# Kernel optimization log

Measured on AMD Instinct MI355X. Metric: run time of the kernel, lower is better.

## Reference

```python
import jax, jax.numpy as jnp
import numpy as np

B, S, E = 2, 2048, 2048
H, DH = 16, 128          # n_head, head_dim
ROT = 32                 # rotary_dim (partial RoPE)
MP = 8                   # mp_num in original forward
MASKED_BIAS = -1e9


def setup_inputs() -> dict:
    key = jax.random.key(0)
    k1, k2, k3 = jax.random.split(key, 3)
    hidden_states = jax.random.normal(k1, (B, S, E), dtype=jnp.float32)
    W_qkv = jax.random.normal(k2, (3 * E, E), dtype=jnp.float32) * (E ** -0.5)
    W_out = jax.random.normal(k3, (E, E), dtype=jnp.float32) * (E ** -0.5)
    return {"hidden_states": hidden_states, "W_qkv": W_qkv, "W_out": W_out}


def _rope_sincos(seq_len, rot_dim, dtype):
    inv_freq = 1.0 / (10000.0 ** (jnp.arange(0, rot_dim, 2, dtype=jnp.float32) / rot_dim))
    ang = jnp.arange(seq_len, dtype=jnp.float32)[:, None] * inv_freq[None, :]  # [S, R/2]
    return jnp.sin(ang).astype(dtype), jnp.cos(ang).astype(dtype)


def _apply_rope(x, sin, cos):
    # x: [B,S,H,R]; sin/cos: [S,R/2] -> repeat_interleave(2) -> [S,R]
    sin2 = jnp.repeat(sin, 2, axis=-1)[None, :, None, :]
    cos2 = jnp.repeat(cos, 2, axis=-1)[None, :, None, :]
    x1 = x[..., ::2]
    x2 = x[..., 1::2]
    rot = jnp.stack((-x2, x1), axis=-1).reshape(x.shape)  # rotate_every_two
    return x * cos2 + rot * sin2


def reference(hidden_states, W_qkv, W_out):
    b, s, e = hidden_states.shape
    # qkv_proj (no bias): torch Linear does x @ W^T
    qkv = jnp.einsum('bse,fe->bsf', hidden_states, W_qkv)          # [B,S,3E]
    qkv = qkv.reshape(b, s, MP, 3 * e // MP)
    q, k, v = jnp.split(qkv, 3, axis=-1)                            # each [B,S,MP,E/MP]
    # _split_heads: flatten mp dim, re-split into heads
    q = q.reshape(b, s, H, DH)
    k = k.reshape(b, s, H, DH)
    v = v.reshape(b, s, H, DH)
    # partial rotary on first ROT dims (q,k in [B,S,H,DH] layout)
    sin, cos = _rope_sincos(s, ROT, hidden_states.dtype)
    q = jnp.concatenate([_apply_rope(q[..., :ROT], sin, cos), q[..., ROT:]], axis=-1)
    k = jnp.concatenate([_apply_rope(k[..., :ROT], sin, cos), k[..., ROT:]], axis=-1)
    # attention: scores / sqrt(DH), causal masked_fill(-1e9), softmax, AV
    scale = jnp.sqrt(jnp.asarray(DH, dtype=jnp.float32)).astype(hidden_states.dtype)
    scores = jnp.einsum('bqhd,bkhd->bhqk', q, k) / scale            # [B,H,S,S]
    causal = jnp.tril(jnp.ones((s, s), dtype=bool))
    scores = jnp.where(causal[None, None], scores, jnp.asarray(MASKED_BIAS, scores.dtype))
    attn = jax.nn.softmax(scores, axis=-1)
    out = jnp.einsum('bhqk,bkhd->bqhd', attn, v)                    # [B,S,H,DH]
    out = out.reshape(b, s, e)
    return jnp.einsum('bse,fe->bsf', out, W_out)                    # out_proj
```

## Files before the change

kernel.cpp:

```cpp
#include <hip/hip_runtime.h>
#include <hip/hip_bf16.h>
#include <cstdint>
#include <cstddef>

using bf16 = __hip_bfloat16;
using short4v = __attribute__((ext_vector_type(4))) short;
using short8 = __attribute__((ext_vector_type(8))) short;
using floatx4 = __attribute__((ext_vector_type(4))) float;

#define MFMA_BF16(A, B, C) __builtin_amdgcn_mfma_f32_16x16x32_bf16((A), (B), (C), 0, 0, 0)

__device__ inline short bf16_bits(float x) {
  bf16 v = __float2bfloat16(x);
  short r;
  __builtin_memcpy(&r, &v, 2);
  return r;
}

__device__ inline void store_c(bf16* p, float v) { *p = __float2bfloat16(v); }
__device__ inline void store_c(float* p, float v) { *p = v; }

__global__ __launch_bounds__(256) void f32_to_bf16_kernel(
    const float* __restrict__ src, bf16* __restrict__ dst, int n8) {
  const int i = blockIdx.x * 256 + threadIdx.x;
  if (i >= n8) return;
  const float4 a = ((const float4*)src)[2 * i];
  const float4 b = ((const float4*)src)[2 * i + 1];
  short8 r;
  r[0] = bf16_bits(a.x); r[1] = bf16_bits(a.y); r[2] = bf16_bits(a.z); r[3] = bf16_bits(a.w);
  r[4] = bf16_bits(b.x); r[5] = bf16_bits(b.y); r[6] = bf16_bits(b.z); r[7] = bf16_bits(b.w);
  *(short8*)(dst + (size_t)i * 8) = r;
}

template <typename TC>
__global__ __launch_bounds__(256) void gemm_bt_async(
    const bf16* __restrict__ A, const bf16* __restrict__ B, TC* __restrict__ C,
    int ldc, int K) {
  __shared__ bf16 As[128 * 64];
  __shared__ bf16 Bs[128 * 64];
  const int tid = threadIdx.x;
  const int lane = tid & 63;
  const int wave = tid >> 6;
  const int lrow = lane & 15;
  const int quad = lane >> 4;
  const int wm = (wave >> 1) * 64;
  const int wn = (wave & 1) * 64;
  const int tm = blockIdx.y * 128;
  const int tn = blockIdx.x * 128;

  const int srow = tid >> 3;
  const int scl = tid & 7;

  floatx4 acc[4][4] = {};

  for (int k0 = 0; k0 < K; k0 += 64) {
    __syncthreads();
#pragma unroll
    for (int r = 0; r < 4; ++r) {
      const int row = r * 32 + srow;
      const int scg = scl ^ (row & 7);
      __builtin_amdgcn_global_load_lds(
          (const __attribute__((address_space(1))) void*)(A + (size_t)(tm + row) * K + k0 + scg * 8),
          (__attribute__((address_space(3))) void*)(As + row * 64 + scl * 8), 16, 0, 0);
    }
#pragma unroll
    for (int r = 0; r < 4; ++r) {
      const int row = r * 32 + srow;
      const int scg = scl ^ (row & 7);
      __builtin_amdgcn_global_load_lds(
          (const __attribute__((address_space(1))) void*)(B + (size_t)(tn + row) * K + k0 + scg * 8),
          (__attribute__((address_space(3))) void*)(Bs + row * 64 + scl * 8), 16, 0, 0);
    }
    __syncthreads();

#pragma unroll
    for (int kk = 0; kk < 2; ++kk) {
      short8 af[4], bfr[4];
#pragma unroll
      for (int i = 0; i < 4; ++i) {
        const int ra = wm + i * 16 + lrow;
        const int rb = wn + i * 16 + lrow;
        af[i] = *(const short8*)&As[ra * 64 + (((kk * 4 + quad) ^ (ra & 7)) * 8)];
        bfr[i] = *(const short8*)&Bs[rb * 64 + (((kk * 4 + quad) ^ (rb & 7)) * 8)];
      }
#pragma unroll
      for (int i = 0; i < 4; ++i)
#pragma unroll
        for (int j = 0; j < 4; ++j)
          acc[i][j] = MFMA_BF16(af[i], bfr[j], acc[i][j]);
    }
  }

#pragma unroll
  for (int i = 0; i < 4; ++i)
#pragma unroll
    for (int j = 0; j < 4; ++j)
#pragma unroll
      for (int r = 0; r < 4; ++r) {
        const int row = tm + wm + i * 16 + quad * 4 + r;
        const int col = tn + wn + j * 16 + lrow;
        store_c(&C[(size_t)row * ldc + col], acc[i][j][r]);
      }
}

__global__ __launch_bounds__(256) void gemm_abf16_bf32(
    const bf16* __restrict__ A, const float* __restrict__ B, float* __restrict__ C,
    int ldc, int K) {
  __shared__ bf16 As[128 * 64];
  __shared__ bf16 Bs[128 * 64];
  const int tid = threadIdx.x;
  const int lane = tid & 63;
  const int wave = tid >> 6;
  const int lrow = lane & 15;
  const int quad = lane >> 4;
  const int wm = (wave >> 1) * 64;
  const int wn = (wave & 1) * 64;
  const int tm = blockIdx.y * 128;
  const int tn = blockIdx.x * 128;

  const int srow = tid >> 3;
  const int scl = tid & 7;
  const int c16 = tid & 15;
  const int br0 = tid >> 4;

  floatx4 acc[4][4] = {};
  float4 breg[8];
#pragma unroll
  for (int r = 0; r < 8; ++r)
    breg[r] = *(const float4*)(B + (size_t)(tn + r * 16 + br0) * K + c16 * 4);

  for (int k0 = 0; k0 < K; k0 += 64) {
    __syncthreads();
#pragma unroll
    for (int r = 0; r < 4; ++r) {
      const int row = r * 32 + srow;
      const int scg = scl ^ (row & 7);
      __builtin_amdgcn_global_load_lds(
          (const __attribute__((address_space(1))) void*)(A + (size_t)(tm + row) * K + k0 + scg * 8),
          (__attribute__((address_space(3))) void*)(As + row * 64 + scl * 8), 16, 0, 0);
    }
#pragma unroll
    for (int r = 0; r < 8; ++r) {
      const int row = r * 16 + br0;
      short4v sv;
      sv[0] = bf16_bits(breg[r].x); sv[1] = bf16_bits(breg[r].y);
      sv[2] = bf16_bits(breg[r].z); sv[3] = bf16_bits(breg[r].w);
      *(short4v*)&Bs[row * 64 + (((c16 >> 1) ^ (row & 7)) * 8) + (c16 & 1) * 4] = sv;
    }
    __syncthreads();
    if (k0 + 64 < K) {
#pragma unroll
      for (int r = 0; r < 8; ++r)
        breg[r] = *(const float4*)(B + (size_t)(tn + r * 16 + br0) * K + k0 + 64 + c16 * 4);
    }

#pragma unroll
    for (int kk = 0; kk < 2; ++kk) {
      short8 af[4], bfr[4];
#pragma unroll
      for (int i = 0; i < 4; ++i) {
        const int ra = wm + i * 16 + lrow;
        const int rb = wn + i * 16 + lrow;
        af[i] = *(const short8*)&As[ra * 64 + (((kk * 4 + quad) ^ (ra & 7)) * 8)];
        bfr[i] = *(const short8*)&Bs[rb * 64 + (((kk * 4 + quad) ^ (rb & 7)) * 8)];
      }
#pragma unroll
      for (int i = 0; i < 4; ++i)
#pragma unroll
        for (int j = 0; j < 4; ++j)
          acc[i][j] = MFMA_BF16(af[i], bfr[j], acc[i][j]);
    }
  }

#pragma unroll
  for (int i = 0; i < 4; ++i)
#pragma unroll
    for (int j = 0; j < 4; ++j)
#pragma unroll
      for (int r = 0; r < 4; ++r) {
        const int row = tm + wm + i * 16 + quad * 4 + r;
        const int col = tn + wn + j * 16 + lrow;
        C[(size_t)row * ldc + col] = acc[i][j][r];
      }
}

__global__ void rope_kernel(bf16* __restrict__ qkv) {
  const int idx = blockIdx.x * 256 + threadIdx.x;
  const int i = idx & 15;
  int t = idx >> 4;
  const int qk = t & 1;
  t >>= 1;
  const int h = t & 15;
  t >>= 4;
  const int s = t & 2047;
  bf16* p = qkv + (size_t)t * 6144 + (h >> 1) * 768 + (h & 1) * 128 + qk * 256 + 2 * i;
  const float x0 = __bfloat162float(p[0]);
  const float x1 = __bfloat162float(p[1]);
  const float inv = powf(10000.f, -(float)(2 * i) / 32.f);
  const float ang = (float)s * inv;
  float sn, cs;
  sincosf(ang, &sn, &cs);
  p[0] = __float2bfloat16(x0 * cs - x1 * sn);
  p[1] = __float2bfloat16(x1 * cs + x0 * sn);
}

__global__ __launch_bounds__(256) void attn_flash_pair(
    const bf16* __restrict__ qkv, bf16* __restrict__ out) {
  __shared__ short Ks[16 * 64 * 8];
  __shared__ short Vs[8 * 128 * 8];
  __shared__ short Ps[8 * 128 * 8];
  const int tid = threadIdx.x;
  const int wave = tid >> 6;
  const int lane = tid & 63;
  const int lq = lane & 15;
  const int quad = lane >> 4;
  const int h = blockIdx.y;
  const int b = blockIdx.z;
  const size_t SROW = 6144;
  const bf16* base = qkv + (size_t)b * 2048 * SROW;
  const int qoff = (h >> 1) * 768 + (h & 1) * 128;
  const int koff = qoff + 256;
  const int voff = qoff + 512;
  const float scale = 0.088388347648318447f;

  const int sr = tid >> 2;
  const int sq = tid & 3;

  const bf16* kbase = base + (size_t)sr * SROW + koff + sq * 32;
  const bf16* vbase = base + (size_t)sr * SROW + voff + sq * 8;

  short8 kv[4], vv[4];
#pragma unroll
  for (int j = 0; j < 4; ++j) kv[j] = *(const short8*)(kbase + j * 8);
#pragma unroll
  for (int i = 0; i < 4; ++i) vv[i] = *(const short8*)(vbase + i * 32);

  for (int phase = 0; phase < 2; ++phase) {
    const int qb = phase ? (15 - (int)blockIdx.x) : (int)blockIdx.x;

    short8 qf[2][4];
#pragma unroll
    for (int rt = 0; rt < 2; ++rt) {
      const bf16* qp =
          base + (size_t)(qb * 128 + wave * 32 + rt * 16 + lq) * SROW + qoff + quad * 8;
#pragma unroll
      for (int ks = 0; ks < 4; ++ks) qf[rt][ks] = *(const short8*)(qp + ks * 32);
    }

    floatx4 o[2][8] = {};
    float m_i[2] = {-1e30f, -1e30f};
    float l_i[2] = {0.f, 0.f};

    const int kb_end = 2 * qb + 2;
    for (int kb = 0; kb < kb_end; ++kb) {
      __syncthreads();

#pragma unroll
      for (int j = 0; j < 4; ++j) *(short8*)&Ks[((sq * 4 + j) * 64 + sr) * 8] = kv[j];
      {
        const int so = (sr >> 3) * 128, si = sr & 7;
#pragma unroll
        for (int i = 0; i < 4; ++i) {
          const int d0 = sq * 8 + i * 32;
#pragma unroll
          for (int j = 0; j < 8; ++j) Vs[(so + d0 + j) * 8 + si] = vv[i][j];
        }
      }
      __syncthreads();

      {
        const bool last = (kb + 1 == kb_end);
        const bool pf = !last || (phase == 0);
        const int nkb = !last ? kb + 1 : 0;
        if (pf) {
          const size_t off = (size_t)nkb * 64 * SROW;
#pragma unroll
          for (int j = 0; j < 4; ++j) kv[j] = *(const short8*)(kbase + off + j * 8);
#pragma unroll
          for (int i = 0; i < 4; ++i) vv[i] = *(const short8*)(vbase + off + i * 32);
        }
      }

      floatx4 sc[2][4] = {};
      __builtin_amdgcn_s_setprio(1);
#pragma unroll
      for (int ks = 0; ks < 4; ++ks) {
        short8 kf[4];
#pragma unroll
        for (int ct = 0; ct < 4; ++ct)
          kf[ct] = *(const short8*)&Ks[((ks * 4 + quad) * 64 + ct * 16 + lq) * 8];
#pragma unroll
        for (int rt = 0; rt < 2; ++rt)
#pragma unroll
          for (int ct = 0; ct < 4; ++ct)
            sc[rt][ct] = MFMA_BF16(kf[ct], qf[rt][ks], sc[rt][ct]);
      }
      __builtin_amdgcn_s_setprio(0);

      const int qrow0 = qb * 128 + wave * 32;
      const bool diag = (kb * 64 + 63 > qrow0);
#pragma unroll
      for (int rt = 0; rt < 2; ++rt) {
        const int qg = qrow0 + rt * 16 + lq;
#pragma unroll
        for (int ct = 0; ct < 4; ++ct)
#pragma unroll
          for (int r = 0; r < 4; ++r) {
            float v = sc[rt][ct][r] * scale;
            if (diag && (kb * 64 + ct * 16 + quad * 4 + r) > qg) v = -1e9f;
            sc[rt][ct][r] = v;
          }
        float c0 = fmaxf(fmaxf(sc[rt][0][0], sc[rt][0][1]), fmaxf(sc[rt][0][2], sc[rt][0][3]));
        float c1 = fmaxf(fmaxf(sc[rt][1][0], sc[rt][1][1]), fmaxf(sc[rt][1][2], sc[rt][1][3]));
        float c2 = fmaxf(fmaxf(sc[rt][2][0], sc[rt][2][1]), fmaxf(sc[rt][2][2], sc[rt][2][3]));
        float c3 = fmaxf(fmaxf(sc[rt][3][0], sc[rt][3][1]), fmaxf(sc[rt][3][2], sc[rt][3][3]));
        float mx = fmaxf(fmaxf(c0, c1), fmaxf(c2, c3));
        mx = fmaxf(mx, __shfl_xor(mx, 16, 64));
        mx = fmaxf(mx, __shfl_xor(mx, 32, 64));
        const float mnew = fmaxf(m_i[rt], mx);
        const float alpha = __expf(m_i[rt] - mnew);
        m_i[rt] = mnew;
        float s0 = 0.f, s1 = 0.f, s2 = 0.f, s3 = 0.f;
#pragma unroll
        for (int ct = 0; ct < 4; ++ct) {
          const float p0 = __expf(sc[rt][ct][0] - mnew);
          const float p1 = __expf(sc[rt][ct][1] - mnew);
          const float p2 = __expf(sc[rt][ct][2] - mnew);
          const float p3 = __expf(sc[rt][ct][3] - mnew);
          sc[rt][ct][0] = p0; sc[rt][ct][1] = p1; sc[rt][ct][2] = p2; sc[rt][ct][3] = p3;
          s0 += p0; s1 += p1; s2 += p2; s3 += p3;
        }
        float rs = (s0 + s1) + (s2 + s3);
        rs += __shfl_xor(rs, 16, 64);
        rs += __shfl_xor(rs, 32, 64);
        l_i[rt] = l_i[rt] * alpha + rs;
#pragma unroll
        for (int dt = 0; dt < 8; ++dt) {
          o[rt][dt][0] *= alpha; o[rt][dt][1] *= alpha;
          o[rt][dt][2] *= alpha; o[rt][dt][3] *= alpha;
        }
        const int prow = wave * 32 + rt * 16 + lq;
#pragma unroll
        for (int ct = 0; ct < 4; ++ct) {
          short4v pv;
          pv[0] = bf16_bits(sc[rt][ct][0]); pv[1] = bf16_bits(sc[rt][ct][1]);
          pv[2] = bf16_bits(sc[rt][ct][2]); pv[3] = bf16_bits(sc[rt][ct][3]);
          const int kgrp = ct * 2 + (quad >> 1);
          *(short4v*)&Ps[(kgrp * 128 + prow) * 8 + (quad & 1) * 4] = pv;
        }
      }

      __builtin_amdgcn_s_setprio(1);
#pragma unroll
      for (int kk = 0; kk < 2; ++kk) {
        short8 pf[2], vf[8];
#pragma unroll
        for (int rt = 0; rt < 2; ++rt)
          pf[rt] = *(const short8*)&Ps[((kk * 4 + quad) * 128 + wave * 32 + rt * 16 + lq) * 8];
#pragma unroll
        for (int dt = 0; dt < 8; ++dt)
          vf[dt] = *(const short8*)&Vs[((kk * 4 + quad) * 128 + dt * 16 + lq) * 8];
#pragma unroll
        for (int rt = 0; rt < 2; ++rt)
#pragma unroll
          for (int dt = 0; dt < 8; ++dt)
            o[rt][dt] = MFMA_BF16(vf[dt], pf[rt], o[rt][dt]);
      }
      __builtin_amdgcn_s_setprio(0);
    }

#pragma unroll
    for (int rt = 0; rt < 2; ++rt) {
      const float inv_l = 1.f / l_i[rt];
      const int qg = qb * 128 + wave * 32 + rt * 16 + lq;
      bf16* op = out + ((size_t)(b * 2048 + qg)) * 2048 + h * 128 + quad * 4;
#pragma unroll
      for (int dt = 0; dt < 8; ++dt) {
        short4v s4;
        s4[0] = bf16_bits(o[rt][dt][0] * inv_l);
        s4[1] = bf16_bits(o[rt][dt][1] * inv_l);
        s4[2] = bf16_bits(o[rt][dt][2] * inv_l);
        s4[3] = bf16_bits(o[rt][dt][3] * inv_l);
        *(short4v*)(op + dt * 16) = s4;
      }
    }
  }
}

extern "C" void kernel_launch(void* const* d_in, const int* in_sizes, int n_in,
                              void* d_out, int out_size, void* d_ws, size_t ws_size,
                              hipStream_t stream) {
  const float* hidden = (const float*)d_in[0];
  const float* Wqkv = (const float*)d_in[1];
  const float* Wout = (const float*)d_in[2];
  float* outp = (float*)d_out;

  bf16* qkv = (bf16*)d_ws;
  bf16* flex = qkv + (size_t)4096 * 6144;
  bf16* hbf = (bf16*)d_out;

  f32_to_bf16_kernel<<<4096, 256, 0, stream>>>(hidden, hbf, 1048576);

  f32_to_bf16_kernel<<<3072, 256, 0, stream>>>(Wqkv, flex, 786432);
  gemm_bt_async<bf16><<<dim3(24, 32), 256, 0, stream>>>(hbf, flex, qkv, 6144, 2048);
  f32_to_bf16_kernel<<<3072, 256, 0, stream>>>(Wqkv + (size_t)3072 * 2048, flex, 786432);
  gemm_bt_async<bf16><<<dim3(24, 32), 256, 0, stream>>>(hbf, flex, qkv + 3072, 6144, 2048);

  rope_kernel<<<8192, 256, 0, stream>>>(qkv);

  bf16* attnout = flex;
  attn_flash_pair<<<dim3(8, 16, 2), 256, 0, stream>>>(qkv, attnout);

  gemm_abf16_bf32<<<dim3(16, 32), 256, 0, stream>>>(attnout, Wout, outp, 2048, 2048);
}
```

Before: 434.8 us.

## Write V transposed from QKV GEMM epilogue and skip no-op softmax rescaling

The QKV projection epilogue now writes the V columns into a separate head-major, transposed buffer ([b,h,d,s]) in the unused half of the output allocation. The attention kernel then loads V rows contiguously and stores them into shared memory with vector stores, replacing the scattered per-element LDS transpose. The online softmax also skips the alpha rescale of the accumulator and the row sum when no lane's max increased, gated by a wave-wide vote. The costs are strided 8-byte global stores in the GEMM epilogue and a divergent branch in the softmax.

Measured after the change: 435.4 us. No clear change (+0.1%).

```diff
diff --git a/kernel.cpp b/kernel.cpp
--- a/kernel.cpp
+++ b/kernel.cpp
@@ -35,7 +35,7 @@
 template <typename TC>
 __global__ __launch_bounds__(256) void gemm_bt_async(
     const bf16* __restrict__ A, const bf16* __restrict__ B, TC* __restrict__ C,
-    int ldc, int K) {
+    int ldc, int K, bf16* __restrict__ vT, int mpbase) {
   __shared__ bf16 As[128 * 64];
   __shared__ bf16 Bs[128 * 64];
   const int tid = threadIdx.x;
@@ -91,16 +91,36 @@
     }
   }
 
-#pragma unroll
-  for (int i = 0; i < 4; ++i)
-#pragma unroll
-    for (int j = 0; j < 4; ++j)
-#pragma unroll
-      for (int r = 0; r < 4; ++r) {
-        const int row = tm + wm + i * 16 + quad * 4 + r;
-        const int col = tn + wn + j * 16 + lrow;
-        store_c(&C[(size_t)row * ldc + col], acc[i][j][r]);
-      }
+  if (vT != nullptr && ((int)blockIdx.x % 6) >= 4) {
+    const int mpl = (int)blockIdx.x / 6;
+#pragma unroll
+    for (int i = 0; i < 4; ++i)
+#pragma unroll
+      for (int j = 0; j < 4; ++j) {
+        const int fl = tn + wn + j * 16 + lrow;
+        const int sv = fl - mpl * 768 - 512;
+        const int hh = mpbase + mpl * 2 + (sv >> 7);
+        const int dd = sv & 127;
+        const int m0 = tm + wm + i * 16 + quad * 4;
+        const int bb = m0 >> 11;
+        const int ss = m0 & 2047;
+        short4v pv;
+        pv[0] = bf16_bits(acc[i][j][0]); pv[1] = bf16_bits(acc[i][j][1]);
+        pv[2] = bf16_bits(acc[i][j][2]); pv[3] = bf16_bits(acc[i][j][3]);
+        *(short4v*)&vT[((size_t)(bb * 16 + hh) * 128 + dd) * 2048 + ss] = pv;
+      }
+  } else {
+#pragma unroll
+    for (int i = 0; i < 4; ++i)
+#pragma unroll
+      for (int j = 0; j < 4; ++j)
+#pragma unroll
+        for (int r = 0; r < 4; ++r) {
+          const int row = tm + wm + i * 16 + quad * 4 + r;
+          const int col = tn + wn + j * 16 + lrow;
+          store_c(&C[(size_t)row * ldc + col], acc[i][j][r]);
+        }
+  }
 }
 
 __global__ __launch_bounds__(256) void gemm_abf16_bf32(
@@ -205,7 +225,8 @@
 }
 
 __global__ __launch_bounds__(256) void attn_flash_pair(
-    const bf16* __restrict__ qkv, bf16* __restrict__ out) {
+    const bf16* __restrict__ qkv, const bf16* __restrict__ vT,
+    bf16* __restrict__ out) {
   __shared__ short Ks[16 * 64 * 8];
   __shared__ short Vs[8 * 128 * 8];
   __shared__ short Ps[8 * 128 * 8];
@@ -220,20 +241,21 @@
   const bf16* base = qkv + (size_t)b * 2048 * SROW;
   const int qoff = (h >> 1) * 768 + (h & 1) * 128;
   const int koff = qoff + 256;
-  const int voff = qoff + 512;
   const float scale = 0.088388347648318447f;
 
   const int sr = tid >> 2;
   const int sq = tid & 3;
-
   const bf16* kbase = base + (size_t)sr * SROW + koff + sq * 32;
-  const bf16* vbase = base + (size_t)sr * SROW + voff + sq * 8;
+
+  const bf16* vrow = vT + (size_t)(b * 16 + h) * 262144 +
+                     (size_t)(tid >> 1) * 2048 + (tid & 1) * 32;
+  short* vdst = &Vs[(((tid & 1) * 4) * 128 + (tid >> 1)) * 8];
 
   short8 kv[4], vv[4];
 #pragma unroll
   for (int j = 0; j < 4; ++j) kv[j] = *(const short8*)(kbase + j * 8);
 #pragma unroll
-  for (int i = 0; i < 4; ++i) vv[i] = *(const short8*)(vbase + i * 32);
+  for (int i = 0; i < 4; ++i) vv[i] = *(const short8*)(vrow + i * 8);
 
   for (int phase = 0; phase < 2; ++phase) {
     const int qb = phase ? (15 - (int)blockIdx.x) : (int)blockIdx.x;
@@ -257,15 +279,8 @@
 
 #pragma unroll
       for (int j = 0; j < 4; ++j) *(short8*)&Ks[((sq * 4 + j) * 64 + sr) * 8] = kv[j];
-      {
-        const int so = (sr >> 3) * 128, si = sr & 7;
-#pragma unroll
-        for (int i = 0; i < 4; ++i) {
-          const int d0 = sq * 8 + i * 32;
-#pragma unroll
-          for (int j = 0; j < 8; ++j) Vs[(so + d0 + j) * 8 + si] = vv[i][j];
-        }
-      }
+#pragma unroll
+      for (int i = 0; i < 4; ++i) *(short8*)(vdst + i * 1024) = vv[i];
       __syncthreads();
 
       {
@@ -273,11 +288,12 @@
         const bool pf = !last || (phase == 0);
         const int nkb = !last ? kb + 1 : 0;
         if (pf) {
-          const size_t off = (size_t)nkb * 64 * SROW;
-#pragma unroll
-          for (int j = 0; j < 4; ++j) kv[j] = *(const short8*)(kbase + off + j * 8);
-#pragma unroll
-          for (int i = 0; i < 4; ++i) vv[i] = *(const short8*)(vbase + off + i * 32);
+          const size_t koffg = (size_t)nkb * 64 * SROW;
+          const int voffg = nkb * 64;
+#pragma unroll
+          for (int j = 0; j < 4; ++j) kv[j] = *(const short8*)(kbase + koffg + j * 8);
+#pragma unroll
+          for (int i = 0; i < 4; ++i) vv[i] = *(const short8*)(vrow + voffg + i * 8);
         }
       }
 
@@ -317,9 +333,15 @@
         float mx = fmaxf(fmaxf(c0, c1), fmaxf(c2, c3));
         mx = fmaxf(mx, __shfl_xor(mx, 16, 64));
         mx = fmaxf(mx, __shfl_xor(mx, 32, 64));
-        const float mnew = fmaxf(m_i[rt], mx);
-        const float alpha = __expf(m_i[rt] - mnew);
-        m_i[rt] = mnew;
+        float mnew = m_i[rt];
+        if (!__all(mx <= mnew)) {
+          mnew = fmaxf(mnew, mx);
+          const float alpha = __expf(m_i[rt] - mnew);
+          m_i[rt] = mnew;
+          l_i[rt] *= alpha;
+#pragma unroll
+          for (int dt = 0; dt < 8; ++dt) o[rt][dt] *= alpha;
+        }
         float s0 = 0.f, s1 = 0.f, s2 = 0.f, s3 = 0.f;
 #pragma unroll
         for (int ct = 0; ct < 4; ++ct) {
@@ -333,12 +355,7 @@
         float rs = (s0 + s1) + (s2 + s3);
         rs += __shfl_xor(rs, 16, 64);
         rs += __shfl_xor(rs, 32, 64);
-        l_i[rt] = l_i[rt] * alpha + rs;
-#pragma unroll
-        for (int dt = 0; dt < 8; ++dt) {
-          o[rt][dt][0] *= alpha; o[rt][dt][1] *= alpha;
-          o[rt][dt][2] *= alpha; o[rt][dt][3] *= alpha;
-        }
+        l_i[rt] += rs;
         const int prow = wave * 32 + rt * 16 + lq;
 #pragma unroll
         for (int ct = 0; ct < 4; ++ct) {
@@ -398,18 +415,19 @@
   bf16* qkv = (bf16*)d_ws;
   bf16* flex = qkv + (size_t)4096 * 6144;
   bf16* hbf = (bf16*)d_out;
+  bf16* vT = (bf16*)d_out + (size_t)8 * 1024 * 1024;
 
   f32_to_bf16_kernel<<<4096, 256, 0, stream>>>(hidden, hbf, 1048576);
 
   f32_to_bf16_kernel<<<3072, 256, 0, stream>>>(Wqkv, flex, 786432);
-  gemm_bt_async<bf16><<<dim3(24, 32), 256, 0, stream>>>(hbf, flex, qkv, 6144, 2048);
+  gemm_bt_async<bf16><<<dim3(24, 32), 256, 0, stream>>>(hbf, flex, qkv, 6144, 2048, vT, 0);
   f32_to_bf16_kernel<<<3072, 256, 0, stream>>>(Wqkv + (size_t)3072 * 2048, flex, 786432);
-  gemm_bt_async<bf16><<<dim3(24, 32), 256, 0, stream>>>(hbf, flex, qkv + 3072, 6144, 2048);
+  gemm_bt_async<bf16><<<dim3(24, 32), 256, 0, stream>>>(hbf, flex, qkv + 3072, 6144, 2048, vT, 8);
 
   rope_kernel<<<8192, 256, 0, stream>>>(qkv);
 
   bf16* attnout = flex;
-  attn_flash_pair<<<dim3(8, 16, 2), 256, 0, stream>>>(qkv, attnout);
+  attn_flash_pair<<<dim3(8, 16, 2), 256, 0, stream>>>(qkv, vT, attnout);
 
   gemm_abf16_bf32<<<dim3(16, 32), 256, 0, stream>>>(attnout, Wout, outp, 2048, 2048);
 }
```
